# Optimization experiments

Hardware: AMD Instinct MI355X
Metric: run time of the kernel (lower is better)

Reference implementation:

```python
import jax, jax.numpy as jnp
import numpy as np

DIM = 768
HEADS = 16
HEAD_DIM = DIM // HEADS  # 48


def setup_inputs() -> dict:
    key = jax.random.key(0)
    ks = jax.random.split(key, 9)
    s = 1.0 / np.sqrt(DIM)
    inp = {
        "x": jax.random.normal(ks[0], (4, 2048, DIM), dtype=jnp.float32),
        "Wq": jax.random.uniform(ks[1], (DIM, DIM), jnp.float32, -s, s),
        "bq": jax.random.uniform(ks[2], (DIM,), jnp.float32, -s, s),
        "Wk": jax.random.uniform(ks[3], (DIM, DIM), jnp.float32, -s, s),
        "bk": jax.random.uniform(ks[4], (DIM,), jnp.float32, -s, s),
        "Wv": jax.random.uniform(ks[5], (DIM, DIM), jnp.float32, -s, s),
        "bv": jax.random.uniform(ks[6], (DIM,), jnp.float32, -s, s),
        "Wo": jax.random.uniform(ks[7], (DIM, DIM), jnp.float32, -s, s),
        "bo": jax.random.uniform(ks[8], (DIM,), jnp.float32, -s, s),
    }
    return inp


def reference(x, Wq, bq, Wk, bk, Wv, bv, Wo, bo):
    B, S, _ = x.shape
    # torch nn.Linear: y = x @ W.T + b
    q = x @ Wq.T + bq
    k = x @ Wk.T + bk
    v = x @ Wv.T + bv
    # split heads: (B, H, S, Dh)
    q = q.reshape(B, S, HEADS, HEAD_DIM).transpose(0, 2, 1, 3)
    k = k.reshape(B, S, HEADS, HEAD_DIM).transpose(0, 2, 1, 3)
    v = v.reshape(B, S, HEADS, HEAD_DIM).transpose(0, 2, 1, 3)
    score = jnp.einsum("bhqd,bhkd->bhqk", q, k) / jnp.sqrt(jnp.float32(HEAD_DIM))
    attn = jax.nn.softmax(score, axis=-1)
    out = jnp.einsum("bhqk,bhkd->bhqd", attn, v)
    out = out.transpose(0, 2, 1, 3).reshape(B, S, DIM)
    return out @ Wo.T + bo
```

## Files before the change

kernel.cpp:

```cpp
#include <hip/hip_runtime.h>

#define DIM 768
#define SEQ 2048
#define NB 4
#define NH 16
#define DH 48
#define DP 64
#define BHN (NB*NH)
#define MTOK (NB*SEQ)

typedef __attribute__((ext_vector_type(8))) short bf16x8;
typedef __attribute__((ext_vector_type(4))) float f32x4;
typedef __attribute__((ext_vector_type(4))) unsigned int u32x4;

__device__ __forceinline__ unsigned short f32_to_bf16(float f) {
    union { float f; unsigned int u; } v; v.f = f;
    unsigned int r = v.u + 0x7fff + ((v.u >> 16) & 1);
    return (unsigned short)(r >> 16);
}

#if __has_builtin(__builtin_amdgcn_exp2f)
#define EXP2F(x) __builtin_amdgcn_exp2f(x)
#else
#define EXP2F(x) exp2f(x)
#endif

#define GL_LDS16(g, l) __builtin_amdgcn_global_load_lds( \
    (const __attribute__((address_space(1))) void*)(g),  \
    (__attribute__((address_space(3))) void*)(l), 16, 0, 0)

__global__ void cvt_all(const float* __restrict__ x,
                        const float* __restrict__ Wq, const float* __restrict__ Wk,
                        const float* __restrict__ Wv, const float* __restrict__ Wo,
                        unsigned short* __restrict__ xb, unsigned short* __restrict__ wb) {
    const int nx = MTOK * DIM;
    const int nw = DIM * DIM;
    int i = (blockIdx.x * blockDim.x + threadIdx.x) * 4;
    const float* src; unsigned short* dst; int off;
    if (i < nx) { src = x; dst = xb; off = i; }
    else {
        int j = i - nx;
        int r = j / nw;
        off = j - r * nw;
        src = (r == 0) ? Wq : (r == 1) ? Wk : (r == 2) ? Wv : Wo;
        dst = wb + r * nw;
    }
    const float4 v = *(const float4*)(src + off);
    ushort4 o;
    o.x = f32_to_bf16(v.x); o.y = f32_to_bf16(v.y);
    o.z = f32_to_bf16(v.z); o.w = f32_to_bf16(v.w);
    *(ushort4*)(dst + off) = o;
}

#define BK 32

__global__ __launch_bounds__(256) void qkv_gemm(
    const unsigned short* __restrict__ xb,
    const unsigned short* __restrict__ wb,
    const float* __restrict__ bq, const float* __restrict__ bk, const float* __restrict__ bv,
    unsigned short* __restrict__ Qb, unsigned short* __restrict__ Kb, unsigned short* __restrict__ Vt)
{
    const int z = blockIdx.z;
    const unsigned short* W = wb + z * (DIM * DIM);
    const float* bias = (z == 0) ? bq : (z == 1) ? bk : bv;
    const int row0 = blockIdx.x * 128;
    const int col0 = blockIdx.y * 128;

    __shared__ __align__(16) short As[128 * BK];
    __shared__ __align__(16) short Bs[128 * BK];

    const int tid = threadIdx.x;
    const int lane = tid & 63;
    const int w = tid >> 6;
    const int wy = w >> 1, wx = w & 1;
    const int l15 = lane & 15, quad = lane >> 4;
    const int lr = lane >> 2;
    const int lco = (lane & 3) * 8;

    f32x4 acc[4][4];
    for (int mi = 0; mi < 4; ++mi) for (int ni = 0; ni < 4; ++ni)
        for (int r = 0; r < 4; ++r) acc[mi][ni][r] = 0.f;

    for (int kt = 0; kt < DIM / BK; ++kt) {
        #pragma unroll
        for (int j = 0; j < 2; ++j) {
            const int c = w * 2 + j;
            GL_LDS16(&xb[(row0 + c * 16 + lr) * DIM + kt * BK + lco], &As[c * 512]);
            GL_LDS16(&W [(col0 + c * 16 + lr) * DIM + kt * BK + lco], &Bs[c * 512]);
        }
        __syncthreads();
        bf16x8 af[4], bfr[4];
        #pragma unroll
        for (int mi = 0; mi < 4; ++mi)
            af[mi] = *(const bf16x8*)&As[(wy * 64 + mi * 16 + l15) * BK + quad * 8];
        #pragma unroll
        for (int ni = 0; ni < 4; ++ni)
            bfr[ni] = *(const bf16x8*)&Bs[(wx * 64 + ni * 16 + l15) * BK + quad * 8];
        if (z == 2) {
            #pragma unroll
            for (int mi = 0; mi < 4; ++mi)
                #pragma unroll
                for (int ni = 0; ni < 4; ++ni)
                    acc[mi][ni] = __builtin_amdgcn_mfma_f32_16x16x32_bf16(af[mi], bfr[ni], acc[mi][ni], 0, 0, 0);
        } else {
            #pragma unroll
            for (int mi = 0; mi < 4; ++mi)
                #pragma unroll
                for (int ni = 0; ni < 4; ++ni)
                    acc[mi][ni] = __builtin_amdgcn_mfma_f32_16x16x32_bf16(bfr[ni], af[mi], acc[mi][ni], 0, 0, 0);
        }
        __syncthreads();
    }

    const float qscale = 0.14433756729740643f * 1.4426950408889634f;

    if (z == 2) {
        #pragma unroll
        for (int mi = 0; mi < 4; ++mi) {
            #pragma unroll
            for (int ni = 0; ni < 4; ++ni) {
                int col = col0 + wx * 64 + ni * 16 + l15;
                int h = col / DH, d = col - h * DH;
                int row = row0 + wy * 64 + mi * 16 + quad * 4;
                int b = row >> 11, s = row & 2047;
                float bi = bias[col];
                union { ushort4 v; unsigned short e[4]; } pk;
                #pragma unroll
                for (int r = 0; r < 4; ++r)
                    pk.e[r] = f32_to_bf16(acc[mi][ni][r] + bi);
                *(ushort4*)&Vt[((b * NH + h) * DP + d) * SEQ + s] = pk.v;
            }
        }
    } else {
        unsigned short* dst = (z == 0) ? Qb : Kb;
        #pragma unroll
        for (int mi = 0; mi < 4; ++mi) {
            int token = row0 + wy * 64 + mi * 16 + l15;
            int b = token >> 11, s = token & 2047;
            #pragma unroll
            for (int ni = 0; ni < 4; ++ni) {
                int f0 = col0 + wx * 64 + ni * 16 + quad * 4;
                const float4 b4 = *(const float4*)&bias[f0];
                int h = f0 / DH, d0 = f0 - h * DH;
                int bh = b * NH + h;
                union { ushort4 v; unsigned short e[4]; } pk;
                if (z == 0) {
                    pk.e[0] = f32_to_bf16((acc[mi][ni][0] + b4.x) * qscale);
                    pk.e[1] = f32_to_bf16((acc[mi][ni][1] + b4.y) * qscale);
                    pk.e[2] = f32_to_bf16((acc[mi][ni][2] + b4.z) * qscale);
                    pk.e[3] = f32_to_bf16((acc[mi][ni][3] + b4.w) * qscale);
                } else {
                    pk.e[0] = f32_to_bf16(acc[mi][ni][0] + b4.x);
                    pk.e[1] = f32_to_bf16(acc[mi][ni][1] + b4.y);
                    pk.e[2] = f32_to_bf16(acc[mi][ni][2] + b4.z);
                    pk.e[3] = f32_to_bf16(acc[mi][ni][3] + b4.w);
                }
                *(ushort4*)&dst[(bh * SEQ + s) * DP + d0] = pk.v;
            }
        }
    }
}

__global__ __launch_bounds__(256) void out_gemm(
    const unsigned short* __restrict__ ab,
    const unsigned short* __restrict__ Wo,
    const float* __restrict__ bo,
    float* __restrict__ out)
{
    const int row0 = blockIdx.x * 128;
    const int col0 = blockIdx.y * 128;

    __shared__ __align__(16) short As[128 * BK];
    __shared__ __align__(16) short Bs[128 * BK];

    const int tid = threadIdx.x;
    const int lane = tid & 63;
    const int w = tid >> 6;
    const int wy = w >> 1, wx = w & 1;
    const int l15 = lane & 15, quad = lane >> 4;
    const int lr = lane >> 2;
    const int lco = (lane & 3) * 8;

    f32x4 acc[4][4];
    for (int mi = 0; mi < 4; ++mi) for (int ni = 0; ni < 4; ++ni)
        for (int r = 0; r < 4; ++r) acc[mi][ni][r] = 0.f;

    for (int kt = 0; kt < DIM / BK; ++kt) {
        #pragma unroll
        for (int j = 0; j < 2; ++j) {
            const int c = w * 2 + j;
            GL_LDS16(&ab[(row0 + c * 16 + lr) * DIM + kt * BK + lco], &As[c * 512]);
            GL_LDS16(&Wo[(col0 + c * 16 + lr) * DIM + kt * BK + lco], &Bs[c * 512]);
        }
        __syncthreads();
        bf16x8 af[4], bfr[4];
        #pragma unroll
        for (int mi = 0; mi < 4; ++mi)
            af[mi] = *(const bf16x8*)&As[(wy * 64 + mi * 16 + l15) * BK + quad * 8];
        #pragma unroll
        for (int ni = 0; ni < 4; ++ni)
            bfr[ni] = *(const bf16x8*)&Bs[(wx * 64 + ni * 16 + l15) * BK + quad * 8];
        #pragma unroll
        for (int mi = 0; mi < 4; ++mi)
            #pragma unroll
            for (int ni = 0; ni < 4; ++ni)
                acc[mi][ni] = __builtin_amdgcn_mfma_f32_16x16x32_bf16(af[mi], bfr[ni], acc[mi][ni], 0, 0, 0);
        __syncthreads();
    }

    #pragma unroll
    for (int mi = 0; mi < 4; ++mi)
        #pragma unroll
        for (int ni = 0; ni < 4; ++ni)
            #pragma unroll
            for (int r = 0; r < 4; ++r) {
                int row = row0 + wy * 64 + mi * 16 + quad * 4 + r;
                int col = col0 + wx * 64 + ni * 16 + l15;
                out[row * DIM + col] = acc[mi][ni][r] + bo[col];
            }
}

__device__ __forceinline__ int keyperm(int a) {
    return (a & 32) + ((a & 12) << 1) + ((a & 16) >> 2) + (a & 3);
}

__global__ __launch_bounds__(256, 2) void attn_kernel(
    const unsigned short* __restrict__ Qb,
    const unsigned short* __restrict__ Kb,
    const unsigned short* __restrict__ Vt,
    unsigned short* __restrict__ Ob)
{
    const int bh = blockIdx.x;
    const int tile = blockIdx.y;
    const int tid = threadIdx.x;
    const int w = tid >> 6;
    const int lane = tid & 63;
    const int l15 = lane & 15, quad = lane >> 4;

    const unsigned short* Qh = Qb + bh * SEQ * DP;
    const unsigned short* Kh = Kb + bh * SEQ * DP;
    const unsigned short* Vh = Vt + bh * DP * SEQ;
    const int q0 = tile * 256 + w * 64;

    __shared__ __align__(16) short Ks[64 * 64];
    __shared__ __align__(16) short Vs[48 * 64];

    bf16x8 aq[4][2];
    #pragma unroll
    for (int m = 0; m < 4; ++m)
        #pragma unroll
        for (int ks = 0; ks < 2; ++ks)
            aq[m][ks] = *(const bf16x8*)&Qh[(q0 + m * 16 + l15) * DP + ks * 32 + quad * 8];
    if (quad >= 2) {
        const bf16x8 z8 = {0, 0, 0, 0, 0, 0, 0, 0};
        #pragma unroll
        for (int m = 0; m < 4; ++m) aq[m][1] = z8;
    }

    f32x4 o[4][3];
    #pragma unroll
    for (int m = 0; m < 4; ++m) for (int ni = 0; ni < 3; ++ni)
        for (int r = 0; r < 4; ++r) o[m][ni][r] = 0.f;
    float ls[4][2];
    #pragma unroll
    for (int m = 0; m < 4; ++m) { ls[m][0] = 0.f; ls[m][1] = 0.f; }

    const f32x4 FZ = {0.f, 0.f, 0.f, 0.f};

    const int sa = tid >> 3;
    const int sc_ = tid & 7;
    const int lc8 = (sc_ ^ (sa & 7)) * 8;
    const int ka0 = keyperm(sa), ka1 = keyperm(sa + 32);
    const int lds_w0 = sa * 64 + sc_ * 8;
    const int lds_w1 = (sa + 32) * 64 + sc_ * 8;
    const bool vsec = (tid < 128);

    bf16x8 kr0, kr1, vr0, vr1;
    kr0 = *(const bf16x8*)&Kh[ka0 * DP + lc8];
    kr1 = *(const bf16x8*)&Kh[ka1 * DP + lc8];
    vr0 = *(const bf16x8*)&Vh[sa * SEQ + lc8];
    if (vsec) vr1 = *(const bf16x8*)&Vh[(sa + 32) * SEQ + lc8];

    for (int kt = 0; kt < SEQ / 64; ++kt) {
        __syncthreads();
        *(bf16x8*)&Ks[lds_w0] = kr0;
        *(bf16x8*)&Ks[lds_w1] = kr1;
        *(bf16x8*)&Vs[lds_w0] = vr0;
        if (vsec) *(bf16x8*)&Vs[lds_w1] = vr1;
        if (kt + 1 < SEQ / 64) {
            const int k0n = (kt + 1) * 64;
            kr0 = *(const bf16x8*)&Kh[(k0n + ka0) * DP + lc8];
            kr1 = *(const bf16x8*)&Kh[(k0n + ka1) * DP + lc8];
            vr0 = *(const bf16x8*)&Vh[sa * SEQ + k0n + lc8];
            if (vsec) vr1 = *(const bf16x8*)&Vh[(sa + 32) * SEQ + k0n + lc8];
        }
        __syncthreads();

        bf16x8 ak0[4], ak1[4];
        #pragma unroll
        for (int n = 0; n < 4; ++n) {
            ak0[n] = *(const bf16x8*)&Ks[(n * 16 + l15) * 64 + ((quad ^ (l15 & 7)) * 8)];
            ak1[n] = *(const bf16x8*)&Ks[(n * 16 + l15) * 64 + (((4 + quad) ^ (l15 & 7)) * 8)];
        }
        bf16x8 av[2][3];
        #pragma unroll
        for (int ks = 0; ks < 2; ++ks)
            #pragma unroll
            for (int mt = 0; mt < 3; ++mt)
                av[ks][mt] = *(const bf16x8*)&Vs[(mt * 16 + l15) * 64 + (((ks * 4 + quad) ^ (l15 & 7)) * 8)];

        #pragma unroll
        for (int mp = 0; mp < 2; ++mp) {
            const int m0 = 2 * mp, m1 = 2 * mp + 1;
            f32x4 sc[2][4];
            #pragma unroll
            for (int n = 0; n < 4; ++n) {
                sc[0][n] = __builtin_amdgcn_mfma_f32_16x16x32_bf16(ak0[n], aq[m0][0], FZ, 0, 0, 0);
                sc[1][n] = __builtin_amdgcn_mfma_f32_16x16x32_bf16(ak0[n], aq[m1][0], FZ, 0, 0, 0);
            }
            #pragma unroll
            for (int n = 0; n < 4; ++n) {
                sc[0][n] = __builtin_amdgcn_mfma_f32_16x16x32_bf16(ak1[n], aq[m0][1], sc[0][n], 0, 0, 0);
                sc[1][n] = __builtin_amdgcn_mfma_f32_16x16x32_bf16(ak1[n], aq[m1][1], sc[1][n], 0, 0, 0);
            }
            union { u32x4 u; bf16x8 h; } bp[2][2];
            #pragma unroll
            for (int mi = 0; mi < 2; ++mi) {
                #pragma unroll
                for (int ks = 0; ks < 2; ++ks) {
                    #pragma unroll
                    for (int w2 = 0; w2 < 4; ++w2) {
                        const int j0 = 2 * w2, j1 = 2 * w2 + 1;
                        float p0 = EXP2F(sc[mi][2 * ks + (j0 >> 2)][j0 & 3]);
                        float p1 = EXP2F(sc[mi][2 * ks + (j1 >> 2)][j1 & 3]);
                        ls[2 * mp + mi][w2 & 1] += (p0 + p1);
                        bp[mi][ks].u[w2] = __builtin_amdgcn_perm(__float_as_uint(p1), __float_as_uint(p0), 0x07060302u);
                    }
                }
            }
            #pragma unroll
            for (int ks = 0; ks < 2; ++ks)
                #pragma unroll
                for (int mt = 0; mt < 3; ++mt) {
                    o[m0][mt] = __builtin_amdgcn_mfma_f32_16x16x32_bf16(av[ks][mt], bp[0][ks].h, o[m0][mt], 0, 0, 0);
                    o[m1][mt] = __builtin_amdgcn_mfma_f32_16x16x32_bf16(av[ks][mt], bp[1][ks].h, o[m1][mt], 0, 0, 0);
                }
        }
    }

    const int b = bh >> 4, h = bh & 15;
    #pragma unroll
    for (int m = 0; m < 4; ++m) {
        float lsum = ls[m][0] + ls[m][1];
        lsum += __shfl_xor(lsum, 16);
        lsum += __shfl_xor(lsum, 32);
        float inv = 1.f / lsum;
        #pragma unroll
        for (int mt = 0; mt < 3; ++mt)
            #pragma unroll
            for (int r = 0; r < 4; ++r) {
                int token = b * SEQ + q0 + m * 16 + l15;
                int d = mt * 16 + quad * 4 + r;
                Ob[token * DIM + h * DH + d] = f32_to_bf16(o[m][mt][r] * inv);
            }
    }
}

extern "C" void kernel_launch(void* const* d_in, const int* in_sizes, int n_in,
                              void* d_out, int out_size, void* d_ws, size_t ws_size,
                              hipStream_t stream) {
    const float* x  = (const float*)d_in[0];
    const float* Wq = (const float*)d_in[1]; const float* bq = (const float*)d_in[2];
    const float* Wk = (const float*)d_in[3]; const float* bk = (const float*)d_in[4];
    const float* Wv = (const float*)d_in[5]; const float* bv = (const float*)d_in[6];
    const float* Wo = (const float*)d_in[7]; const float* bo = (const float*)d_in[8];

    unsigned char* ws = (unsigned char*)d_ws;
    unsigned short* xb = (unsigned short*)(ws);
    unsigned short* wb = (unsigned short*)(ws + 12582912);
    unsigned short* Qb = (unsigned short*)(ws + 17301504);
    unsigned short* Kb = (unsigned short*)(ws + 34078720);
    unsigned short* Vt = (unsigned short*)(ws + 50855936);
    unsigned short* Ob = (unsigned short*)(ws + 67633152);

    cvt_all<<<8448, 256, 0, stream>>>(x, Wq, Wk, Wv, Wo, xb, wb);

    qkv_gemm<<<dim3(MTOK / 128, DIM / 128, 3), 256, 0, stream>>>(xb, wb, bq, bk, bv, Qb, Kb, Vt);
    attn_kernel<<<dim3(BHN, SEQ / 256), 256, 0, stream>>>(Qb, Kb, Vt, Ob);
    out_gemm<<<dim3(MTOK / 128, DIM / 128), 256, 0, stream>>>(Ob, wb + 3 * DIM * DIM, bo, (float*)d_out);
}
```

Before: 241.6 us.

## Double attention key tile to 128 and revert QK projection epilogue to scalar stores

The attention kernel now stages 128 keys per iteration instead of 64, with V loaded as 16-column rows. This halves the number of block-wide barriers and iterations and gives each thread more prefetched loads in flight, at the cost of more LDS and more registers per thread. Separately, the Q/K projection drops its swapped-operand MFMA path and vectorized ushort4 stores in favour of uniform MFMA ordering with per-element scalar bf16 stores, which makes global writes less coalesced.

```diff
diff --git a/kernel.cpp b/kernel.cpp
--- a/kernel.cpp
+++ b/kernel.cpp
@@ -96,19 +96,11 @@
         #pragma unroll
         for (int ni = 0; ni < 4; ++ni)
             bfr[ni] = *(const bf16x8*)&Bs[(wx * 64 + ni * 16 + l15) * BK + quad * 8];
-        if (z == 2) {
-            #pragma unroll
-            for (int mi = 0; mi < 4; ++mi)
-                #pragma unroll
-                for (int ni = 0; ni < 4; ++ni)
-                    acc[mi][ni] = __builtin_amdgcn_mfma_f32_16x16x32_bf16(af[mi], bfr[ni], acc[mi][ni], 0, 0, 0);
-        } else {
-            #pragma unroll
-            for (int mi = 0; mi < 4; ++mi)
-                #pragma unroll
-                for (int ni = 0; ni < 4; ++ni)
-                    acc[mi][ni] = __builtin_amdgcn_mfma_f32_16x16x32_bf16(bfr[ni], af[mi], acc[mi][ni], 0, 0, 0);
-        }
+        #pragma unroll
+        for (int mi = 0; mi < 4; ++mi)
+            #pragma unroll
+            for (int ni = 0; ni < 4; ++ni)
+                acc[mi][ni] = __builtin_amdgcn_mfma_f32_16x16x32_bf16(af[mi], bfr[ni], acc[mi][ni], 0, 0, 0);
         __syncthreads();
     }
 
@@ -132,30 +124,21 @@
             }
         }
     } else {
-        unsigned short* dst = (z == 0) ? Qb : Kb;
         #pragma unroll
         for (int mi = 0; mi < 4; ++mi) {
-            int token = row0 + wy * 64 + mi * 16 + l15;
-            int b = token >> 11, s = token & 2047;
             #pragma unroll
             for (int ni = 0; ni < 4; ++ni) {
-                int f0 = col0 + wx * 64 + ni * 16 + quad * 4;
-                const float4 b4 = *(const float4*)&bias[f0];
-                int h = f0 / DH, d0 = f0 - h * DH;
-                int bh = b * NH + h;
-                union { ushort4 v; unsigned short e[4]; } pk;
-                if (z == 0) {
-                    pk.e[0] = f32_to_bf16((acc[mi][ni][0] + b4.x) * qscale);
-                    pk.e[1] = f32_to_bf16((acc[mi][ni][1] + b4.y) * qscale);
-                    pk.e[2] = f32_to_bf16((acc[mi][ni][2] + b4.z) * qscale);
-                    pk.e[3] = f32_to_bf16((acc[mi][ni][3] + b4.w) * qscale);
-                } else {
-                    pk.e[0] = f32_to_bf16(acc[mi][ni][0] + b4.x);
-                    pk.e[1] = f32_to_bf16(acc[mi][ni][1] + b4.y);
-                    pk.e[2] = f32_to_bf16(acc[mi][ni][2] + b4.z);
-                    pk.e[3] = f32_to_bf16(acc[mi][ni][3] + b4.w);
+                #pragma unroll
+                for (int r = 0; r < 4; ++r) {
+                    int row = row0 + wy * 64 + mi * 16 + quad * 4 + r;
+                    int col = col0 + wx * 64 + ni * 16 + l15;
+                    float v = acc[mi][ni][r] + bias[col];
+                    int b = row >> 11, s = row & 2047;
+                    int h = col / DH, d = col - h * DH;
+                    int bh = b * NH + h;
+                    if (z == 0) Qb[(bh * SEQ + s) * DP + d] = f32_to_bf16(v * qscale);
+                    else        Kb[(bh * SEQ + s) * DP + d] = f32_to_bf16(v);
                 }
-                *(ushort4*)&dst[(bh * SEQ + s) * DP + d0] = pk.v;
             }
         }
     }
@@ -219,6 +202,8 @@
                 out[row * DIM + col] = acc[mi][ni][r] + bo[col];
             }
 }
+
+#define KT 128
 
 __device__ __forceinline__ int keyperm(int a) {
     return (a & 32) + ((a & 12) << 1) + ((a & 16) >> 2) + (a & 3);
@@ -242,8 +227,8 @@
     const unsigned short* Vh = Vt + bh * DP * SEQ;
     const int q0 = tile * 256 + w * 64;
 
-    __shared__ __align__(16) short Ks[64 * 64];
-    __shared__ __align__(16) short Vs[48 * 64];
+    __shared__ __align__(16) short Ks[KT * 64];
+    __shared__ __align__(16) short Vs[48 * KT];
 
     bf16x8 aq[4][2];
     #pragma unroll
@@ -271,80 +256,92 @@
     const int sc_ = tid & 7;
     const int lc8 = (sc_ ^ (sa & 7)) * 8;
     const int ka0 = keyperm(sa), ka1 = keyperm(sa + 32);
-    const int lds_w0 = sa * 64 + sc_ * 8;
-    const int lds_w1 = (sa + 32) * 64 + sc_ * 8;
-    const bool vsec = (tid < 128);
-
-    bf16x8 kr0, kr1, vr0, vr1;
-    kr0 = *(const bf16x8*)&Kh[ka0 * DP + lc8];
-    kr1 = *(const bf16x8*)&Kh[ka1 * DP + lc8];
-    vr0 = *(const bf16x8*)&Vh[sa * SEQ + lc8];
-    if (vsec) vr1 = *(const bf16x8*)&Vh[(sa + 32) * SEQ + lc8];
-
-    for (int kt = 0; kt < SEQ / 64; ++kt) {
-        __syncthreads();
-        *(bf16x8*)&Ks[lds_w0] = kr0;
-        *(bf16x8*)&Ks[lds_w1] = kr1;
-        *(bf16x8*)&Vs[lds_w0] = vr0;
-        if (vsec) *(bf16x8*)&Vs[lds_w1] = vr1;
-        if (kt + 1 < SEQ / 64) {
-            const int k0n = (kt + 1) * 64;
+    const int rv = tid >> 4;
+    const int cv = tid & 15;
+    const int lcv = (cv ^ (rv & 7)) * 8;
+
+    bf16x8 kr0, kr1, kr2, kr3, vr0, vr1, vr2;
+    kr0 = *(const bf16x8*)&Kh[(ka0) * DP + lc8];
+    kr1 = *(const bf16x8*)&Kh[(ka1) * DP + lc8];
+    kr2 = *(const bf16x8*)&Kh[(64 + ka0) * DP + lc8];
+    kr3 = *(const bf16x8*)&Kh[(64 + ka1) * DP + lc8];
+    vr0 = *(const bf16x8*)&Vh[(rv) * SEQ + lcv];
+    vr1 = *(const bf16x8*)&Vh[(rv + 16) * SEQ + lcv];
+    vr2 = *(const bf16x8*)&Vh[(rv + 32) * SEQ + lcv];
+
+    for (int kt = 0; kt < SEQ / KT; ++kt) {
+        __syncthreads();
+        *(bf16x8*)&Ks[(sa) * 64 + sc_ * 8]      = kr0;
+        *(bf16x8*)&Ks[(sa + 32) * 64 + sc_ * 8] = kr1;
+        *(bf16x8*)&Ks[(sa + 64) * 64 + sc_ * 8] = kr2;
+        *(bf16x8*)&Ks[(sa + 96) * 64 + sc_ * 8] = kr3;
+        *(bf16x8*)&Vs[(rv) * KT + cv * 8]       = vr0;
+        *(bf16x8*)&Vs[(rv + 16) * KT + cv * 8]  = vr1;
+        *(bf16x8*)&Vs[(rv + 32) * KT + cv * 8]  = vr2;
+        if (kt + 1 < SEQ / KT) {
+            const int k0n = (kt + 1) * KT;
             kr0 = *(const bf16x8*)&Kh[(k0n + ka0) * DP + lc8];
             kr1 = *(const bf16x8*)&Kh[(k0n + ka1) * DP + lc8];
-            vr0 = *(const bf16x8*)&Vh[sa * SEQ + k0n + lc8];
-            if (vsec) vr1 = *(const bf16x8*)&Vh[(sa + 32) * SEQ + k0n + lc8];
-        }
-        __syncthreads();
-
-        bf16x8 ak0[4], ak1[4];
-        #pragma unroll
-        for (int n = 0; n < 4; ++n) {
-            ak0[n] = *(const bf16x8*)&Ks[(n * 16 + l15) * 64 + ((quad ^ (l15 & 7)) * 8)];
-            ak1[n] = *(const bf16x8*)&Ks[(n * 16 + l15) * 64 + (((4 + quad) ^ (l15 & 7)) * 8)];
-        }
-        bf16x8 av[2][3];
-        #pragma unroll
-        for (int ks = 0; ks < 2; ++ks)
-            #pragma unroll
-            for (int mt = 0; mt < 3; ++mt)
-                av[ks][mt] = *(const bf16x8*)&Vs[(mt * 16 + l15) * 64 + (((ks * 4 + quad) ^ (l15 & 7)) * 8)];
-
-        #pragma unroll
-        for (int mp = 0; mp < 2; ++mp) {
-            const int m0 = 2 * mp, m1 = 2 * mp + 1;
-            f32x4 sc[2][4];
+            kr2 = *(const bf16x8*)&Kh[(k0n + 64 + ka0) * DP + lc8];
+            kr3 = *(const bf16x8*)&Kh[(k0n + 64 + ka1) * DP + lc8];
+            vr0 = *(const bf16x8*)&Vh[(rv) * SEQ + k0n + lcv];
+            vr1 = *(const bf16x8*)&Vh[(rv + 16) * SEQ + k0n + lcv];
+            vr2 = *(const bf16x8*)&Vh[(rv + 32) * SEQ + k0n + lcv];
+        }
+        __syncthreads();
+
+        #pragma unroll
+        for (int hh = 0; hh < 2; ++hh) {
+            bf16x8 ak0[4], ak1[4];
             #pragma unroll
             for (int n = 0; n < 4; ++n) {
-                sc[0][n] = __builtin_amdgcn_mfma_f32_16x16x32_bf16(ak0[n], aq[m0][0], FZ, 0, 0, 0);
-                sc[1][n] = __builtin_amdgcn_mfma_f32_16x16x32_bf16(ak0[n], aq[m1][0], FZ, 0, 0, 0);
-            }
-            #pragma unroll
-            for (int n = 0; n < 4; ++n) {
-                sc[0][n] = __builtin_amdgcn_mfma_f32_16x16x32_bf16(ak1[n], aq[m0][1], sc[0][n], 0, 0, 0);
-                sc[1][n] = __builtin_amdgcn_mfma_f32_16x16x32_bf16(ak1[n], aq[m1][1], sc[1][n], 0, 0, 0);
-            }
-            union { u32x4 u; bf16x8 h; } bp[2][2];
-            #pragma unroll
-            for (int mi = 0; mi < 2; ++mi) {
-                #pragma unroll
-                for (int ks = 0; ks < 2; ++ks) {
+                ak0[n] = *(const bf16x8*)&Ks[(hh * 64 + n * 16 + l15) * 64 + ((quad ^ (l15 & 7)) * 8)];
+                ak1[n] = *(const bf16x8*)&Ks[(hh * 64 + n * 16 + l15) * 64 + (((4 + quad) ^ (l15 & 7)) * 8)];
+            }
+            bf16x8 av[2][3];
+            #pragma unroll
+            for (int ks = 0; ks < 2; ++ks)
+                #pragma unroll
+                for (int mt = 0; mt < 3; ++mt)
+                    av[ks][mt] = *(const bf16x8*)&Vs[(mt * 16 + l15) * KT + ((hh * 8 + ((ks * 4 + quad) ^ (l15 & 7))) * 8)];
+
+            #pragma unroll
+            for (int mp = 0; mp < 2; ++mp) {
+                const int m0 = 2 * mp, m1 = 2 * mp + 1;
+                f32x4 sc[2][4];
+                #pragma unroll
+                for (int n = 0; n < 4; ++n) {
+                    sc[0][n] = __builtin_amdgcn_mfma_f32_16x16x32_bf16(ak0[n], aq[m0][0], FZ, 0, 0, 0);
+                    sc[1][n] = __builtin_amdgcn_mfma_f32_16x16x32_bf16(ak0[n], aq[m1][0], FZ, 0, 0, 0);
+                }
+                #pragma unroll
+                for (int n = 0; n < 4; ++n) {
+                    sc[0][n] = __builtin_amdgcn_mfma_f32_16x16x32_bf16(ak1[n], aq[m0][1], sc[0][n], 0, 0, 0);
+                    sc[1][n] = __builtin_amdgcn_mfma_f32_16x16x32_bf16(ak1[n], aq[m1][1], sc[1][n], 0, 0, 0);
+                }
+                union { u32x4 u; bf16x8 h; } bp[2][2];
+                #pragma unroll
+                for (int mi = 0; mi < 2; ++mi) {
                     #pragma unroll
-                    for (int w2 = 0; w2 < 4; ++w2) {
-                        const int j0 = 2 * w2, j1 = 2 * w2 + 1;
-                        float p0 = EXP2F(sc[mi][2 * ks + (j0 >> 2)][j0 & 3]);
-                        float p1 = EXP2F(sc[mi][2 * ks + (j1 >> 2)][j1 & 3]);
-                        ls[2 * mp + mi][w2 & 1] += (p0 + p1);
-                        bp[mi][ks].u[w2] = __builtin_amdgcn_perm(__float_as_uint(p1), __float_as_uint(p0), 0x07060302u);
+                    for (int ks = 0; ks < 2; ++ks) {
+                        #pragma unroll
+                        for (int w2 = 0; w2 < 4; ++w2) {
+                            const int j0 = 2 * w2, j1 = 2 * w2 + 1;
+                            float p0 = EXP2F(sc[mi][2 * ks + (j0 >> 2)][j0 & 3]);
+                            float p1 = EXP2F(sc[mi][2 * ks + (j1 >> 2)][j1 & 3]);
+                            ls[2 * mp + mi][w2 & 1] += (p0 + p1);
+                            bp[mi][ks].u[w2] = __builtin_amdgcn_perm(__float_as_uint(p1), __float_as_uint(p0), 0x07060302u);
+                        }
                     }
                 }
-            }
-            #pragma unroll
-            for (int ks = 0; ks < 2; ++ks)
-                #pragma unroll
-                for (int mt = 0; mt < 3; ++mt) {
-                    o[m0][mt] = __builtin_amdgcn_mfma_f32_16x16x32_bf16(av[ks][mt], bp[0][ks].h, o[m0][mt], 0, 0, 0);
-                    o[m1][mt] = __builtin_amdgcn_mfma_f32_16x16x32_bf16(av[ks][mt], bp[1][ks].h, o[m1][mt], 0, 0, 0);
-                }
+                #pragma unroll
+                for (int ks = 0; ks < 2; ++ks)
+                    #pragma unroll
+                    for (int mt = 0; mt < 3; ++mt) {
+                        o[m0][mt] = __builtin_amdgcn_mfma_f32_16x16x32_bf16(av[ks][mt], bp[0][ks].h, o[m0][mt], 0, 0, 0);
+                        o[m1][mt] = __builtin_amdgcn_mfma_f32_16x16x32_bf16(av[ks][mt], bp[1][ks].h, o[m1][mt], 0, 0, 0);
+                    }
+            }
         }
     }
 
```

After: 274.0 us. 1.13x slower.
